# Kernel optimization log

Hardware: AMD Instinct MI355X
Metric: run time of the kernel (lower is better)

Reference implementation:

```python
import jax, jax.numpy as jnp
import numpy as np

B, T, D_IN = 16, 4096, 512
D_EMB, N_CODES = 256, 1024


def setup_inputs() -> dict:
    key = jax.random.key(0)
    k1, k2, k3, k4 = jax.random.split(key, 4)
    z = jax.random.normal(k1, (B, T, D_IN), dtype=jnp.float32)
    embedding = jax.random.normal(k2, (N_CODES, D_EMB), dtype=jnp.float32)
    # torch Linear weight layout [out_features, in_features], bias=False
    proj_down_w = jax.random.normal(k3, (D_EMB, D_IN), dtype=jnp.float32) * (1.0 / np.sqrt(D_IN))
    proj_up_w = jax.random.normal(k4, (D_IN, D_EMB), dtype=jnp.float32) * (1.0 / np.sqrt(D_EMB))
    return {"z": z, "embedding": embedding, "proj_down_w": proj_down_w, "proj_up_w": proj_up_w}


def _quantize_to_code(z_e, codebook):
    # z_e: [b, t, d]; codebook: [n, d] -> indices [b, t]
    b, t, d = z_e.shape
    z_flat = z_e.reshape(b * t, d)
    dist = (jnp.sum(z_flat * z_flat, axis=1, keepdims=True)
            - 2.0 * (z_flat @ codebook.T)
            + jnp.sum(codebook * codebook, axis=1)[None, :])  # [(b t), n]
    return jnp.argmin(dist, axis=1).reshape(b, t)


def reference(z, embedding, proj_down_w, proj_up_w):
    # proj_down: z @ W_down^T
    z_e = jnp.einsum('btd,ed->bte', z, proj_down_w)  # [b, t, D_EMB]
    code = _quantize_to_code(z_e, embedding)
    z_q = embedding[code]  # gather: [b, t, D_EMB]
    diff2 = (z_q - z_e) ** 2
    commitment_loss = diff2.mean(axis=(1, 2))  # [b]
    codebook_loss = diff2.mean(axis=(1, 2))    # [b] (same values fwd; differ in grad)
    # straight-through estimator (training mode)
    z_q_st = z_e + jax.lax.stop_gradient(z_q - z_e)
    z_q_out = jnp.einsum('bte,de->btd', z_q_st, proj_up_w)  # [b, t, D_IN]
    return (z_q_out, commitment_loss, codebook_loss, code, z_e)
```

## Files before the change

kernel.cpp:

```cpp
#include <hip/hip_runtime.h>
#include <stdint.h>

#define DIN  512
#define DE   256
#define NC   1024
#define M_   65536
#define FLAGCAP 16384

typedef unsigned short u16;
typedef __attribute__((ext_vector_type(8))) short short8_t;
typedef __attribute__((ext_vector_type(4))) float f32x4_t;
typedef __attribute__((ext_vector_type(16))) float f32x16_t;

__device__ __forceinline__ float bf2f(u16 u) {
    unsigned x = ((unsigned)u) << 16; return __builtin_bit_cast(float, x);
}
__device__ __forceinline__ u16 f2bf(float f) {
    unsigned x = __builtin_bit_cast(unsigned, f);
    x += 0x7fffu + ((x >> 16) & 1u);
    return (u16)(x >> 16);
}
__device__ __forceinline__ void cvt8_hl(float4 a, float4 b, short8_t& h, short8_t& l) {
    float v[8] = {a.x,a.y,a.z,a.w, b.x,b.y,b.z,b.w};
#pragma unroll
    for (int j = 0; j < 8; ++j) {
        u16 hh = f2bf(v[j]);
        h[j] = (short)hh; l[j] = (short)f2bf(v[j] - bf2f(hh));
    }
}
__device__ __forceinline__ short8_t cvt8(float4 a, float4 b) {
    float v[8] = {a.x,a.y,a.z,a.w, b.x,b.y,b.z,b.w};
    short8_t h;
#pragma unroll
    for (int j = 0; j < 8; ++j) h[j] = (short)f2bf(v[j]);
    return h;
}

__global__ void k_init(const float* __restrict__ emb, const float* __restrict__ Wd,
                       u16* __restrict__ embH, u16* __restrict__ embL,
                       u16* __restrict__ WdH,  u16* __restrict__ WdL,
                       float* __restrict__ cnorm, float* __restrict__ rownorm,
                       float* __restrict__ lossacc, int* __restrict__ flagcnt) {
    int tid = blockIdx.x * 256 + threadIdx.x;
    for (int i = tid; i < DE * DIN; i += 65536) {
        float v = Wd[i]; u16 h = f2bf(v);
        WdH[i] = h; WdL[i] = f2bf(v - bf2f(h));
    }
    for (int i = tid; i < NC * DE; i += 65536) {
        float v = emb[i]; u16 h = f2bf(v);
        embH[i] = h; embL[i] = f2bf(v - bf2f(h));
    }
    if (tid < M_) rownorm[tid] = 0.f;
    if (tid < NC) {
        const float* c = emb + (size_t)tid * DE;
        double s = 0.0;
        for (int j = 0; j < DE; ++j) { double v = c[j]; s += v * v; }
        cnorm[tid] = (float)s;
    }
    if (tid < 16) lossacc[tid] = 0.f;
    if (tid == 16) *flagcnt = 0;
}

__global__ __launch_bounds__(512) void k_ze(
        const float* __restrict__ Z,
        const u16* __restrict__ WdH, const u16* __restrict__ WdL,
        float* __restrict__ zeF, float* __restrict__ rownorm) {
    __shared__ __align__(16) u16 aH[2][128 * 40];
    __shared__ __align__(16) u16 aL[2][128 * 40];
    const int bz = blockIdx.x >> 1, mh = blockIdx.x & 1;
    const int t = threadIdx.x, lane = t & 63, wv = t >> 6;
    const int lr = lane & 15, lg = lane >> 4;
    const int zrow = bz * 128 + wv * 16 + lr;
    const int mbase = mh * 128;
    const int srow = t >> 2, skseg = (t & 3) * 8;

#define STAGE_WD(kt_, b_) { \
        size_t off = (size_t)(mbase + srow) * DIN + (kt_) * 32 + skseg; \
        uint4 vh = *(const uint4*)(WdH + off); \
        uint4 vl = *(const uint4*)(WdL + off); \
        *(uint4*)&aH[b_][srow * 40 + skseg] = vh; \
        *(uint4*)&aL[b_][srow * 40 + skseg] = vl; }

    f32x4_t acc[8];
#pragma unroll
    for (int i = 0; i < 8; ++i) acc[i] = (f32x4_t){0.f, 0.f, 0.f, 0.f};

    STAGE_WD(0, 0);
#pragma unroll
    for (int kt = 0; kt < 16; ++kt) {
        __syncthreads();
        if (kt < 15) STAGE_WD(kt + 1, (kt + 1) & 1);
        const float4* zp = (const float4*)(Z + (size_t)zrow * DIN + kt * 32 + lg * 8);
        short8_t bh, bl; cvt8_hl(zp[0], zp[1], bh, bl);
        const int buf = kt & 1;
#pragma unroll
        for (int mi = 0; mi < 8; ++mi) {
            short8_t ah = *(const short8_t*)&aH[buf][(mi * 16 + lr) * 40 + lg * 8];
            short8_t al = *(const short8_t*)&aL[buf][(mi * 16 + lr) * 40 + lg * 8];
            acc[mi] = __builtin_amdgcn_mfma_f32_16x16x32_bf16(ah, bh, acc[mi], 0, 0, 0);
            acc[mi] = __builtin_amdgcn_mfma_f32_16x16x32_bf16(ah, bl, acc[mi], 0, 0, 0);
            acc[mi] = __builtin_amdgcn_mfma_f32_16x16x32_bf16(al, bh, acc[mi], 0, 0, 0);
        }
    }
#undef STAGE_WD
    float rn = 0.f;
#pragma unroll
    for (int mi = 0; mi < 8; ++mi) {
        f32x4_t v = acc[mi];
        rn += v[0]*v[0] + v[1]*v[1] + v[2]*v[2] + v[3]*v[3];
        *(f32x4_t*)(zeF + (size_t)zrow * DE + mbase + mi * 16 + lg * 4) = v;
    }
    rn += __shfl_xor(rn, 16, 64);
    rn += __shfl_xor(rn, 32, 64);
    if (lane < 16) atomicAdd(&rownorm[zrow], rn);
}

__global__ __launch_bounds__(256, 2) void k_argmin(
        const float* __restrict__ zeF,
        const u16* __restrict__ embH, const u16* __restrict__ embL,
        const float* __restrict__ cnorm, const float* __restrict__ rownorm,
        u16* __restrict__ codew, int* __restrict__ flaglist,
        int* __restrict__ flagcnt, float* __restrict__ lossacc) {
    __shared__ __align__(16) u16 aH[2][128 * 40];
    __shared__ __align__(16) u16 aL[2][128 * 40];
    __shared__ float lCn[NC];
    __shared__ float lLoss[128];
    const int m0 = blockIdx.x * 128;
    const int t = threadIdx.x, lane = t & 63, wv = t >> 6;
    const int lc = lane & 31, hi = lane >> 5;
    const int zrow = m0 + wv * 32 + lc;

    for (int i = t; i < NC; i += 256) lCn[i] = cnorm[i];

    short8_t bh[16], bl[16];
#pragma unroll
    for (int c = 0; c < 16; ++c) {
        const float4* zp = (const float4*)(zeF + (size_t)zrow * DE + c * 16 + hi * 8);
        cvt8_hl(zp[0], zp[1], bh[c], bl[c]);
    }

#define STAGE_E(ct_, kt_, b_) { \
        _Pragma("unroll") \
        for (int j = 0; j < 2; ++j) { \
            int idx = t + j * 256; \
            int row = idx >> 2, seg = (idx & 3) * 8; \
            size_t off = (size_t)((ct_) * 128 + row) * DE + (kt_) * 32 + seg; \
            uint4 vh = *(const uint4*)(embH + off); \
            uint4 vl = *(const uint4*)(embL + off); \
            *(uint4*)&aH[b_][row * 40 + seg] = vh; \
            *(uint4*)&aL[b_][row * 40 + seg] = vl; \
        } }

    float best = 3.4e38f, sec = 3.4e38f; int bidx = 0;
    STAGE_E(0, 0, 0);
    for (int ct = 0; ct < 8; ++ct) {
        f32x16_t acc[4];
#pragma unroll
        for (int s = 0; s < 4; ++s)
#pragma unroll
            for (int r = 0; r < 16; ++r) acc[s][r] = 0.f;
#pragma unroll
        for (int kt = 0; kt < 8; ++kt) {
            __syncthreads();
            if (kt < 7)      STAGE_E(ct, kt + 1, (kt + 1) & 1)
            else if (ct < 7) STAGE_E(ct + 1, 0, 0)
            const int buf = kt & 1;
#pragma unroll
            for (int ks = 0; ks < 2; ++ks) {
                const int c = kt * 2 + ks;
#pragma unroll
                for (int s = 0; s < 4; ++s) {
                    short8_t ah = *(const short8_t*)&aH[buf][(s * 32 + lc) * 40 + ks * 16 + hi * 8];
                    short8_t al = *(const short8_t*)&aL[buf][(s * 32 + lc) * 40 + ks * 16 + hi * 8];
                    acc[s] = __builtin_amdgcn_mfma_f32_32x32x16_bf16(ah, bh[c], acc[s], 0, 0, 0);
                    acc[s] = __builtin_amdgcn_mfma_f32_32x32x16_bf16(ah, bl[c], acc[s], 0, 0, 0);
                    acc[s] = __builtin_amdgcn_mfma_f32_32x32x16_bf16(al, bh[c], acc[s], 0, 0, 0);
                }
            }
        }
#pragma unroll
        for (int s = 0; s < 4; ++s)
#pragma unroll
            for (int r = 0; r < 16; ++r) {
                const int cidx = ct * 128 + s * 32 + (r & 3) + 8 * (r >> 2) + 4 * hi;
                float d = fmaf(-2.f, acc[s][r], lCn[cidx]);
                bool lt = d < best;
                sec  = lt ? best : fminf(sec, d);
                best = lt ? d : best;
                bidx = lt ? cidx : bidx;
            }
    }
#undef STAGE_E
    {
        float ob = __shfl_xor(best, 32, 64);
        float os = __shfl_xor(sec,  32, 64);
        int   oi = __shfl_xor(bidx, 32, 64);
        float ns = fminf(fminf(sec, os), fmaxf(best, ob));
        if (ob < best) { best = ob; bidx = oi; }
        sec = ns;
    }
    if (lane < 32) {
        codew[zrow] = (u16)bidx;
        if (sec - best < 0.02f) {
            int pos = atomicAdd(flagcnt, 1);
            if (pos < FLAGCAP) flaglist[pos] = zrow;
        }
        lLoss[wv * 32 + lc] = rownorm[zrow] + best;
    }
    __syncthreads();
    for (int str = 64; str > 0; str >>= 1) {
        if (t < str) lLoss[t] += lLoss[t + str];
        __syncthreads();
    }
    if (t == 0) atomicAdd(&lossacc[m0 >> 12], lLoss[0]);
}

__global__ __launch_bounds__(256) void k_refine(
        const float* __restrict__ Z, const float* __restrict__ Wd,
        const float* __restrict__ emb,
        const int* __restrict__ flaglist, const int* __restrict__ flagcnt,
        u16* __restrict__ codew) {
    __shared__ float  lz[DIN];
    __shared__ double lze[DE];
    __shared__ double ld[256];
    __shared__ int    li[256];
    int n = *flagcnt; if (n < 0) n = 0; if (n > FLAGCAP) n = FLAGCAP;
    int t = threadIdx.x;
    for (int f = blockIdx.x; f < n; f += gridDim.x) {
        int row = flaglist[f] & (M_ - 1);
        __syncthreads();
        for (int i = t; i < DIN; i += 256) lz[i] = Z[(size_t)row * DIN + i];
        __syncthreads();
        double a = 0.0;
        const float* wr = Wd + (size_t)t * DIN;
        for (int k = 0; k < DIN; ++k) a += (double)lz[k] * (double)wr[k];
        lze[t] = a;
        __syncthreads();
        double bd = 1e300; int bi = 0;
        for (int cc = 0; cc < 4; ++cc) {
            int c = cc * 256 + t;
            const float* cr = emb + (size_t)c * DE;
            double s = 0.0;
            for (int e = 0; e < DE; ++e) {
                double diff = lze[e] - (double)cr[e];
                s += diff * diff;
            }
            if (s < bd) { bd = s; bi = c; }
        }
        ld[t] = bd; li[t] = bi;
        __syncthreads();
        for (int str = 128; str > 0; str >>= 1) {
            if (t < str) {
                double od = ld[t + str]; int oi = li[t + str];
                if (od < ld[t] || (od == ld[t] && oi < li[t])) { ld[t] = od; li[t] = oi; }
            }
            __syncthreads();
        }
        if (t == 0) codew[row] = (u16)li[0];
        __syncthreads();
    }
}

__global__ void k_loss(const float* __restrict__ lossacc,
                       float* __restrict__ out_commit, float* __restrict__ out_codebook) {
    int tid = threadIdx.x;
    if (tid < 16) {
        float v = lossacc[tid] * (1.f / 1048576.f);
        out_commit[tid] = v; out_codebook[tid] = v;
    }
}
__global__ void k_codef(const u16* __restrict__ codew, float* __restrict__ out_code) {
    int tid = blockIdx.x * 256 + threadIdx.x;
    if (tid < M_) out_code[tid] = (float)(codew[tid] & (NC - 1));
}

__global__ __launch_bounds__(512) void k_gemm3(
        const float* __restrict__ emb, const float* __restrict__ Wu,
        const float* __restrict__ out_code, float* __restrict__ out) {
    __shared__ __align__(16) u16 gA[128 * 264];
    const int bz = blockIdx.x >> 1, nh = blockIdx.x & 1;
    const int m0 = bz * 128;
    const int t = threadIdx.x, lane = t & 63, wv = t >> 6;
    const int lr = lane & 15, lg = lane >> 4;
    {
        const int row = t >> 2, seg = (t & 3) * 64;
        const int code = (int)out_code[m0 + row] & (NC - 1);
        const float* src = emb + (size_t)code * DE + seg;
#pragma unroll
        for (int j = 0; j < 8; ++j) {
            const float4* p = (const float4*)(src + j * 8);
            *(short8_t*)&gA[row * 264 + seg + j * 8] = cvt8(p[0], p[1]);
        }
    }
    __syncthreads();

    const int nbase = nh * 256 + wv * 32;
    f32x4_t acc[8][2];
#pragma unroll
    for (int i = 0; i < 8; ++i)
#pragma unroll
        for (int j = 0; j < 2; ++j) acc[i][j] = (f32x4_t){0.f, 0.f, 0.f, 0.f};

#pragma unroll
    for (int kt = 0; kt < 8; ++kt) {
        const int k0 = kt * 32 + lg * 8;
        short8_t b0, b1;
        {
            const float4* p = (const float4*)(Wu + (size_t)(nbase + lr) * DE + k0);
            b0 = cvt8(p[0], p[1]);
            const float4* q = (const float4*)(Wu + (size_t)(nbase + 16 + lr) * DE + k0);
            b1 = cvt8(q[0], q[1]);
        }
#pragma unroll
        for (int mi = 0; mi < 8; ++mi) {
            short8_t a = *(const short8_t*)&gA[(mi * 16 + lr) * 264 + k0];
            acc[mi][0] = __builtin_amdgcn_mfma_f32_16x16x32_bf16(a, b0, acc[mi][0], 0, 0, 0);
            acc[mi][1] = __builtin_amdgcn_mfma_f32_16x16x32_bf16(a, b1, acc[mi][1], 0, 0, 0);
        }
    }
#pragma unroll
    for (int mi = 0; mi < 8; ++mi)
#pragma unroll
        for (int reg = 0; reg < 4; ++reg) {
            const int zr = m0 + mi * 16 + lg * 4 + reg;
            out[(size_t)zr * DIN + nbase + lr]      = acc[mi][0][reg];
            out[(size_t)zr * DIN + nbase + 16 + lr] = acc[mi][1][reg];
        }
}

extern "C" void kernel_launch(void* const* d_in, const int* in_sizes, int n_in,
                              void* d_out, int out_size, void* d_ws, size_t ws_size,
                              hipStream_t stream) {
    const float* Z   = (const float*)d_in[0];
    const float* E   = (const float*)d_in[1];
    const float* Wd  = (const float*)d_in[2];
    const float* Wu  = (const float*)d_in[3];

    float* out       = (float*)d_out;
    float* out_zq    = out;
    float* out_com   = out + 33554432;
    float* out_cb    = out + 33554448;
    float* out_code  = out + 33554464;
    float* out_ze    = out + 33620000;

    char* scr = (char*)d_out;
    u16*   embH     = (u16*)  (scr + 0);
    u16*   embL     = (u16*)  (scr + 524288);
    u16*   WdH      = (u16*)  (scr + 1048576);
    u16*   WdL      = (u16*)  (scr + 1310720);
    float* cnorm    = (float*)(scr + 1572864);
    float* rownorm  = (float*)(scr + 1576960);
    u16*   codew    = (u16*)  (scr + 1839104);
    int*   flaglist = (int*)  (scr + 1970176);
    int*   flagcnt  = (int*)  (scr + 2035712);
    float* lossacc  = (float*)(scr + 2035776);
    (void)d_ws; (void)ws_size; (void)in_sizes; (void)n_in; (void)out_size;

    k_init  <<<256,  256, 0, stream>>>(E, Wd, embH, embL, WdH, WdL, cnorm,
                                       rownorm, lossacc, flagcnt);
    k_ze    <<<1024, 512, 0, stream>>>(Z, WdH, WdL, out_ze, rownorm);
    k_argmin<<<512,  256, 0, stream>>>(out_ze, embH, embL, cnorm, rownorm,
                                       codew, flaglist, flagcnt, lossacc);
    k_refine<<<128,  256, 0, stream>>>(Z, Wd, E, flaglist, flagcnt, codew);
    k_loss  <<<1,    64,  0, stream>>>(lossacc, out_com, out_cb);
    k_codef <<<256,  256, 0, stream>>>(codew, out_code);
    k_gemm3 <<<1024, 512, 0, stream>>>(E, Wu, out_code, out_zq);
}
```

Before: 389.0 us.

## Fuse down-projection GEMM into argmin kernel and register-stage shared-memory prefetch

Merges the z_e projection kernel into the argmin kernel. Each block now computes its 128 rows of z_e across all 256 embedding columns with 32x32 MFMA tiles and computes row norms in registers, so the rownorm buffer and its atomics are gone. Global loads for the next stage are now held in registers and written to shared memory after the MFMAs, which overlaps load latency with compute. The cost is a much larger accumulator footprint (8 f32x16 tiles), which raises register pressure under the 2-blocks-per-CU launch bound. z_e is still written to global and read back for the argmin step.

```diff
diff --git a/kernel.cpp b/kernel.cpp
--- a/kernel.cpp
+++ b/kernel.cpp
@@ -39,7 +39,7 @@
 __global__ void k_init(const float* __restrict__ emb, const float* __restrict__ Wd,
                        u16* __restrict__ embH, u16* __restrict__ embL,
                        u16* __restrict__ WdH,  u16* __restrict__ WdL,
-                       float* __restrict__ cnorm, float* __restrict__ rownorm,
+                       float* __restrict__ cnorm,
                        float* __restrict__ lossacc, int* __restrict__ flagcnt) {
     int tid = blockIdx.x * 256 + threadIdx.x;
     for (int i = tid; i < DE * DIN; i += 65536) {
@@ -50,7 +50,6 @@
         float v = emb[i]; u16 h = f2bf(v);
         embH[i] = h; embL[i] = f2bf(v - bf2f(h));
     }
-    if (tid < M_) rownorm[tid] = 0.f;
     if (tid < NC) {
         const float* c = emb + (size_t)tid * DE;
         double s = 0.0;
@@ -61,64 +60,12 @@
     if (tid == 16) *flagcnt = 0;
 }
 
-__global__ __launch_bounds__(512) void k_ze(
+__global__ __launch_bounds__(256, 2) void k_fused(
         const float* __restrict__ Z,
         const u16* __restrict__ WdH, const u16* __restrict__ WdL,
-        float* __restrict__ zeF, float* __restrict__ rownorm) {
-    __shared__ __align__(16) u16 aH[2][128 * 40];
-    __shared__ __align__(16) u16 aL[2][128 * 40];
-    const int bz = blockIdx.x >> 1, mh = blockIdx.x & 1;
-    const int t = threadIdx.x, lane = t & 63, wv = t >> 6;
-    const int lr = lane & 15, lg = lane >> 4;
-    const int zrow = bz * 128 + wv * 16 + lr;
-    const int mbase = mh * 128;
-    const int srow = t >> 2, skseg = (t & 3) * 8;
-
-#define STAGE_WD(kt_, b_) { \
-        size_t off = (size_t)(mbase + srow) * DIN + (kt_) * 32 + skseg; \
-        uint4 vh = *(const uint4*)(WdH + off); \
-        uint4 vl = *(const uint4*)(WdL + off); \
-        *(uint4*)&aH[b_][srow * 40 + skseg] = vh; \
-        *(uint4*)&aL[b_][srow * 40 + skseg] = vl; }
-
-    f32x4_t acc[8];
-#pragma unroll
-    for (int i = 0; i < 8; ++i) acc[i] = (f32x4_t){0.f, 0.f, 0.f, 0.f};
-
-    STAGE_WD(0, 0);
-#pragma unroll
-    for (int kt = 0; kt < 16; ++kt) {
-        __syncthreads();
-        if (kt < 15) STAGE_WD(kt + 1, (kt + 1) & 1);
-        const float4* zp = (const float4*)(Z + (size_t)zrow * DIN + kt * 32 + lg * 8);
-        short8_t bh, bl; cvt8_hl(zp[0], zp[1], bh, bl);
-        const int buf = kt & 1;
-#pragma unroll
-        for (int mi = 0; mi < 8; ++mi) {
-            short8_t ah = *(const short8_t*)&aH[buf][(mi * 16 + lr) * 40 + lg * 8];
-            short8_t al = *(const short8_t*)&aL[buf][(mi * 16 + lr) * 40 + lg * 8];
-            acc[mi] = __builtin_amdgcn_mfma_f32_16x16x32_bf16(ah, bh, acc[mi], 0, 0, 0);
-            acc[mi] = __builtin_amdgcn_mfma_f32_16x16x32_bf16(ah, bl, acc[mi], 0, 0, 0);
-            acc[mi] = __builtin_amdgcn_mfma_f32_16x16x32_bf16(al, bh, acc[mi], 0, 0, 0);
-        }
-    }
-#undef STAGE_WD
-    float rn = 0.f;
-#pragma unroll
-    for (int mi = 0; mi < 8; ++mi) {
-        f32x4_t v = acc[mi];
-        rn += v[0]*v[0] + v[1]*v[1] + v[2]*v[2] + v[3]*v[3];
-        *(f32x4_t*)(zeF + (size_t)zrow * DE + mbase + mi * 16 + lg * 4) = v;
-    }
-    rn += __shfl_xor(rn, 16, 64);
-    rn += __shfl_xor(rn, 32, 64);
-    if (lane < 16) atomicAdd(&rownorm[zrow], rn);
-}
-
-__global__ __launch_bounds__(256, 2) void k_argmin(
-        const float* __restrict__ zeF,
         const u16* __restrict__ embH, const u16* __restrict__ embL,
-        const float* __restrict__ cnorm, const float* __restrict__ rownorm,
+        const float* __restrict__ cnorm,
+        float* __restrict__ zeF,
         u16* __restrict__ codew, int* __restrict__ flaglist,
         int* __restrict__ flagcnt, float* __restrict__ lossacc) {
     __shared__ __align__(16) u16 aH[2][128 * 40];
@@ -132,6 +79,84 @@
 
     for (int i = t; i < NC; i += 256) lCn[i] = cnorm[i];
 
+    const int srow = t >> 1, sseg = (t & 1) * 16;
+    const float* Zrow = Z + (size_t)zrow * DIN;
+
+    uint4 qh[2][2], ql[2][2];
+#define WD_LOAD(kt_) { \
+    _Pragma("unroll") for (int b = 0; b < 2; ++b) { \
+        size_t off = (size_t)(b * 128 + srow) * DIN + (size_t)(kt_) * 32 + sseg; \
+        qh[b][0] = *(const uint4*)(WdH + off); qh[b][1] = *(const uint4*)(WdH + off + 8); \
+        ql[b][0] = *(const uint4*)(WdL + off); ql[b][1] = *(const uint4*)(WdL + off + 8); } }
+#define WD_WRITE() { \
+    _Pragma("unroll") for (int b = 0; b < 2; ++b) { \
+        *(uint4*)&aH[b][srow * 40 + sseg]     = qh[b][0]; \
+        *(uint4*)&aH[b][srow * 40 + sseg + 8] = qh[b][1]; \
+        *(uint4*)&aL[b][srow * 40 + sseg]     = ql[b][0]; \
+        *(uint4*)&aL[b][srow * 40 + sseg + 8] = ql[b][1]; } }
+#define Z_LOAD(kt_, d_) { \
+        const float4* zp = (const float4*)(Zrow + (kt_) * 32 + hi * 8); \
+        d_[0] = zp[0]; d_[1] = zp[1]; \
+        const float4* zq = (const float4*)(Zrow + (kt_) * 32 + 16 + hi * 8); \
+        d_[2] = zq[0]; d_[3] = zq[1]; }
+
+    float4 zr[4], zn[4];
+    Z_LOAD(0, zr);
+    WD_LOAD(0);
+    WD_WRITE();
+    __syncthreads();
+
+    f32x16_t acc[8];
+#pragma unroll
+    for (int s = 0; s < 8; ++s)
+#pragma unroll
+        for (int r = 0; r < 16; ++r) acc[s][r] = 0.f;
+
+    for (int kt = 0; kt < 16; ++kt) {
+        if (kt < 15) { WD_LOAD(kt + 1); Z_LOAD(kt + 1, zn); }
+        short8_t zh0, zl0, zh1, zl1;
+        cvt8_hl(zr[0], zr[1], zh0, zl0);
+        cvt8_hl(zr[2], zr[3], zh1, zl1);
+#pragma unroll
+        for (int ks = 0; ks < 2; ++ks) {
+            short8_t zbh = ks ? zh1 : zh0, zbl = ks ? zl1 : zl0;
+#pragma unroll
+            for (int s = 0; s < 8; ++s) {
+                const int lo = ((s & 3) * 32 + lc) * 40 + ks * 16 + hi * 8;
+                short8_t ah = *(const short8_t*)&aH[s >> 2][lo];
+                short8_t al = *(const short8_t*)&aL[s >> 2][lo];
+                acc[s] = __builtin_amdgcn_mfma_f32_32x32x16_bf16(ah, zbh, acc[s], 0, 0, 0);
+                acc[s] = __builtin_amdgcn_mfma_f32_32x32x16_bf16(ah, zbl, acc[s], 0, 0, 0);
+                acc[s] = __builtin_amdgcn_mfma_f32_32x32x16_bf16(al, zbh, acc[s], 0, 0, 0);
+            }
+        }
+        if (kt < 15) {
+            __syncthreads();
+            WD_WRITE();
+            zr[0] = zn[0]; zr[1] = zn[1]; zr[2] = zn[2]; zr[3] = zn[3];
+            __syncthreads();
+        }
+    }
+#undef WD_LOAD
+#undef WD_WRITE
+#undef Z_LOAD
+
+    float rn = 0.f;
+#pragma unroll
+    for (int s = 0; s < 8; ++s)
+#pragma unroll
+        for (int r = 0; r < 16; ++r) rn += acc[s][r] * acc[s][r];
+    rn += __shfl_xor(rn, 32, 64);
+#pragma unroll
+    for (int s = 0; s < 8; ++s)
+#pragma unroll
+        for (int q = 0; q < 4; ++q) {
+            float4 v = {acc[s][q * 4 + 0], acc[s][q * 4 + 1],
+                        acc[s][q * 4 + 2], acc[s][q * 4 + 3]};
+            *(float4*)(zeF + (size_t)zrow * DE + s * 32 + q * 8 + hi * 4) = v;
+        }
+    __syncthreads();
+
     short8_t bh[16], bl[16];
 #pragma unroll
     for (int c = 0; c < 16; ++c) {
@@ -139,58 +164,63 @@
         cvt8_hl(zp[0], zp[1], bh[c], bl[c]);
     }
 
-#define STAGE_E(ct_, kt_, b_) { \
-        _Pragma("unroll") \
-        for (int j = 0; j < 2; ++j) { \
-            int idx = t + j * 256; \
-            int row = idx >> 2, seg = (idx & 3) * 8; \
-            size_t off = (size_t)((ct_) * 128 + row) * DE + (kt_) * 32 + seg; \
-            uint4 vh = *(const uint4*)(embH + off); \
-            uint4 vl = *(const uint4*)(embL + off); \
-            *(uint4*)&aH[b_][row * 40 + seg] = vh; \
-            *(uint4*)&aL[b_][row * 40 + seg] = vl; \
-        } }
+    uint4 ph[2], pl[2];
+#define STAGE_LOAD(ct_, kt_) { \
+    _Pragma("unroll") for (int j = 0; j < 2; ++j) { \
+        int idx = t + j * 256; int row = idx >> 2, seg = (idx & 3) * 8; \
+        size_t off = (size_t)((ct_) * 128 + row) * DE + (size_t)(kt_) * 32 + seg; \
+        ph[j] = *(const uint4*)(embH + off); \
+        pl[j] = *(const uint4*)(embL + off); } }
+#define STAGE_WRITE(b_) { \
+    _Pragma("unroll") for (int j = 0; j < 2; ++j) { \
+        int idx = t + j * 256; int row = idx >> 2, seg = (idx & 3) * 8; \
+        *(uint4*)&aH[b_][row * 40 + seg] = ph[j]; \
+        *(uint4*)&aL[b_][row * 40 + seg] = pl[j]; } }
 
     float best = 3.4e38f, sec = 3.4e38f; int bidx = 0;
-    STAGE_E(0, 0, 0);
+    STAGE_LOAD(0, 0); STAGE_WRITE(0);
     for (int ct = 0; ct < 8; ++ct) {
-        f32x16_t acc[4];
+        f32x16_t ac2[4];
 #pragma unroll
         for (int s = 0; s < 4; ++s)
 #pragma unroll
-            for (int r = 0; r < 16; ++r) acc[s][r] = 0.f;
+            for (int r = 0; r < 16; ++r) ac2[s][r] = 0.f;
 #pragma unroll
         for (int kt = 0; kt < 8; ++kt) {
             __syncthreads();
-            if (kt < 7)      STAGE_E(ct, kt + 1, (kt + 1) & 1)
-            else if (ct < 7) STAGE_E(ct + 1, 0, 0)
+            const bool pf = (kt < 7) || (ct < 7);
+            if (kt < 7)      { STAGE_LOAD(ct, kt + 1) }
+            else if (ct < 7) { STAGE_LOAD(ct + 1, 0) }
             const int buf = kt & 1;
 #pragma unroll
             for (int ks = 0; ks < 2; ++ks) {
                 const int c = kt * 2 + ks;
 #pragma unroll
                 for (int s = 0; s < 4; ++s) {
-                    short8_t ah = *(const short8_t*)&aH[buf][(s * 32 + lc) * 40 + ks * 16 + hi * 8];
-                    short8_t al = *(const short8_t*)&aL[buf][(s * 32 + lc) * 40 + ks * 16 + hi * 8];
-                    acc[s] = __builtin_amdgcn_mfma_f32_32x32x16_bf16(ah, bh[c], acc[s], 0, 0, 0);
-                    acc[s] = __builtin_amdgcn_mfma_f32_32x32x16_bf16(ah, bl[c], acc[s], 0, 0, 0);
-                    acc[s] = __builtin_amdgcn_mfma_f32_32x32x16_bf16(al, bh[c], acc[s], 0, 0, 0);
+                    const int lo = (s * 32 + lc) * 40 + ks * 16 + hi * 8;
+                    short8_t ah = *(const short8_t*)&aH[buf][lo];
+                    short8_t al = *(const short8_t*)&aL[buf][lo];
+                    ac2[s] = __builtin_amdgcn_mfma_f32_32x32x16_bf16(ah, bh[c], ac2[s], 0, 0, 0);
+                    ac2[s] = __builtin_amdgcn_mfma_f32_32x32x16_bf16(ah, bl[c], ac2[s], 0, 0, 0);
+                    ac2[s] = __builtin_amdgcn_mfma_f32_32x32x16_bf16(al, bh[c], ac2[s], 0, 0, 0);
                 }
             }
+            if (pf) { STAGE_WRITE((kt + 1) & 1) }
         }
 #pragma unroll
         for (int s = 0; s < 4; ++s)
 #pragma unroll
             for (int r = 0; r < 16; ++r) {
                 const int cidx = ct * 128 + s * 32 + (r & 3) + 8 * (r >> 2) + 4 * hi;
-                float d = fmaf(-2.f, acc[s][r], lCn[cidx]);
+                float d = fmaf(-2.f, ac2[s][r], lCn[cidx]);
                 bool lt = d < best;
                 sec  = lt ? best : fminf(sec, d);
                 best = lt ? d : best;
                 bidx = lt ? cidx : bidx;
             }
     }
-#undef STAGE_E
+#undef STAGE_LOAD
+#undef STAGE_WRITE
     {
         float ob = __shfl_xor(best, 32, 64);
         float os = __shfl_xor(sec,  32, 64);
@@ -205,7 +235,7 @@
             int pos = atomicAdd(flagcnt, 1);
             if (pos < FLAGCAP) flaglist[pos] = zrow;
         }
-        lLoss[wv * 32 + lc] = rownorm[zrow] + best;
+        lLoss[wv * 32 + lc] = rn + best;
     }
     __syncthreads();
     for (int str = 64; str > 0; str >>= 1) {
@@ -349,20 +379,18 @@
     u16*   WdH      = (u16*)  (scr + 1048576);
     u16*   WdL      = (u16*)  (scr + 1310720);
     float* cnorm    = (float*)(scr + 1572864);
-    float* rownorm  = (float*)(scr + 1576960);
     u16*   codew    = (u16*)  (scr + 1839104);
     int*   flaglist = (int*)  (scr + 1970176);
     int*   flagcnt  = (int*)  (scr + 2035712);
     float* lossacc  = (float*)(scr + 2035776);
     (void)d_ws; (void)ws_size; (void)in_sizes; (void)n_in; (void)out_size;
 
-    k_init  <<<256,  256, 0, stream>>>(E, Wd, embH, embL, WdH, WdL, cnorm,
-                                       rownorm, lossacc, flagcnt);
-    k_ze    <<<1024, 512, 0, stream>>>(Z, WdH, WdL, out_ze, rownorm);
-    k_argmin<<<512,  256, 0, stream>>>(out_ze, embH, embL, cnorm, rownorm,
-                                       codew, flaglist, flagcnt, lossacc);
-    k_refine<<<128,  256, 0, stream>>>(Z, Wd, E, flaglist, flagcnt, codew);
-    k_loss  <<<1,    64,  0, stream>>>(lossacc, out_com, out_cb);
-    k_codef <<<256,  256, 0, stream>>>(codew, out_code);
-    k_gemm3 <<<1024, 512, 0, stream>>>(E, Wu, out_code, out_zq);
-}
+    k_init  <<<256, 256, 0, stream>>>(E, Wd, embH, embL, WdH, WdL, cnorm,
+                                      lossacc, flagcnt);
+    k_fused <<<512, 256, 0, stream>>>(Z, WdH, WdL, embH, embL, cnorm, out_ze,
+                                      codew, flaglist, flagcnt, lossacc);
+    k_refine<<<128, 256, 0, stream>>>(Z, Wd, E, flaglist, flagcnt, codew);
+    k_loss  <<<1,   64,  0, stream>>>(lossacc, out_com, out_cb);
+    k_codef <<<256, 256, 0, stream>>>(codew, out_code);
+    k_gemm3 <<<1024,512, 0, stream>>>(E, Wu, out_code, out_zq);
+}
```

New measurement: 448.1 us. +15.2%, slower.
